# Performance work log

Measured on AMD Instinct MI355X. Metric: run time of the kernel, lower is better.

Reference implementation:

```python
import jax, jax.numpy as jnp
import numpy as np

B, S, D = 4, 2048, 768
H = 12
HD = D // H  # 64
SCALE = HD ** -0.5

def setup_inputs() -> dict:
    key = jax.random.key(0)
    k1, k2, k3 = jax.random.split(key, 3)
    x = jax.random.normal(k1, (B, S, D), dtype=jnp.float32)
    w_qkv = jax.random.normal(k2, (D, 3 * D), dtype=jnp.float32) * (D ** -0.5)
    w_out = jax.random.normal(k3, (D, D), dtype=jnp.float32) * (D ** -0.5)
    b_out = jnp.zeros((D,), dtype=jnp.float32)
    return {"x": x, "w_qkv": w_qkv, "w_out": w_out, "b_out": b_out}

def reference(x, w_qkv, w_out, b_out):
    B_, S_, D_ = x.shape
    # qkv projection (no bias), then 'b s (qkv h d) -> qkv b h s d'
    qkv = (x @ w_qkv).reshape(B_, S_, 3, H, HD).transpose(2, 0, 3, 1, 4)
    q, k, v = qkv[0], qkv[1], qkv[2]  # each [B, H, S, HD]
    att = jnp.einsum('bhxd,bhyd->bhxy', q, k) * SCALE
    att = jax.nn.softmax(att, axis=-1)  # dropout_rate=0 -> identity
    out = jnp.einsum('bhxy,bhyd->bhxd', att, v)
    out = out.transpose(0, 2, 1, 3).reshape(B_, S_, D_)  # 'b h s d -> b s (h d)'
    return out @ w_out + b_out
```

## Files before the change

### kernel.cpp

```cpp
#include <hip/hip_runtime.h>

#define BB 4
#define SS 2048
#define DD 768
#define HH 12
#define HDIM 64

using bf16_t = __bf16;
typedef __bf16 bf16x8 __attribute__((ext_vector_type(8)));
typedef __bf16 bf16x4 __attribute__((ext_vector_type(4)));
typedef float f32x4 __attribute__((ext_vector_type(4)));
typedef unsigned int u32;

static __device__ __forceinline__ void cp16(void* lds, const void* g) {
  __builtin_amdgcn_global_load_lds(
      (const __attribute__((address_space(1))) u32*)g,
      (__attribute__((address_space(3))) u32*)lds, 16, 0, 0);
}

__global__ void cvt_x(const float* __restrict__ in, bf16_t* __restrict__ out) {
  const size_t i = ((size_t)blockIdx.x * 256 + threadIdx.x) * 8;
  f32x4 f0 = *(const f32x4*)(in + i);
  f32x4 f1 = *(const f32x4*)(in + i + 4);
  bf16x8 v;
#pragma unroll
  for (int j = 0; j < 4; j++) { v[j] = (bf16_t)f0[j]; v[4 + j] = (bf16_t)f1[j]; }
  *(bf16x8*)(out + i) = v;
}

__global__ void wt_transpose(const float* __restrict__ in, bf16_t* __restrict__ out,
                             int K, int N) {
  __shared__ bf16_t tile[64][65];
  const int n0 = blockIdx.x * 64, k0 = blockIdx.y * 64;
  const int t = threadIdx.x;
  const int r = t >> 2;
  const int c0 = (t & 3) * 16;
  const float* src = in + (size_t)(k0 + r) * N + n0 + c0;
#pragma unroll
  for (int q = 0; q < 4; q++) {
    f32x4 f = *(const f32x4*)(src + q * 4);
#pragma unroll
    for (int j = 0; j < 4; j++) tile[r][c0 + q * 4 + j] = (bf16_t)f[j];
  }
  __syncthreads();
  bf16x8 o0, o1;
#pragma unroll
  for (int j = 0; j < 8; j++) { o0[j] = tile[c0 + j][r]; o1[j] = tile[c0 + 8 + j][r]; }
  *(bf16x8*)(out + (size_t)(n0 + r) * K + k0 + c0) = o0;
  *(bf16x8*)(out + (size_t)(n0 + r) * K + k0 + c0 + 8) = o1;
}

template <int MODE>
__global__ __launch_bounds__(256, 2)
void gemm_bt(const bf16_t* __restrict__ A, const bf16_t* __restrict__ Bt,
             int M, int N, int K,
             bf16_t* __restrict__ q_out, bf16_t* __restrict__ k_out,
             bf16_t* __restrict__ vt_out,
             float* __restrict__ Cout, const float* __restrict__ bias) {
  __shared__ bf16_t As[2][128][64];
  __shared__ bf16_t Bs[2][128][64];
  const int t = threadIdx.x;
  const int lane = t & 63, wave = t >> 6;
  const int l15 = lane & 15, quad = lane >> 4;
  const int wm = (wave >> 1) * 64, wn = (wave & 1) * 64;

  const int nx = gridDim.x;
  const int L = blockIdx.y * nx + blockIdx.x;
  const int chunk = (nx * gridDim.y) >> 3;
  const int v = (L & 7) * chunk + (L >> 3);
  const int m0 = (v / nx) * 128, n0 = (v % nx) * 128;

  const int srow = lane >> 3;
  const int schunk = ((lane & 7) ^ srow) * 8;
  const int rsw = l15 & 7;

  f32x4 acc[4][4];
#pragma unroll
  for (int i = 0; i < 4; i++)
#pragma unroll
    for (int j = 0; j < 4; j++) acc[i][j] = (f32x4){0.f, 0.f, 0.f, 0.f};

  auto stage = [&](int k0, int buf) {
#pragma unroll
    for (int p = 0; p < 4; p++) {
      const int row = wave * 32 + p * 8 + srow;
      const bf16_t* asrc;
      if (MODE == 0) {
        asrc = A + (size_t)(m0 + row) * K + k0 + schunk;
      } else {
        const int mm = m0 + row, b = mm >> 11, s = mm & 2047, h = k0 >> 6;
        asrc = A + (((size_t)(b * HH + h)) * SS + s) * HDIM + schunk;
      }
      cp16(&As[buf][wave * 32 + p * 8][0], asrc);
      cp16(&Bs[buf][wave * 32 + p * 8][0],
           Bt + (size_t)(n0 + row) * K + k0 + schunk);
    }
  };

  const int NT = K / 64;
  stage(0, 0);

  for (int kt = 0; kt < NT; kt++) {
    const int buf = kt & 1;
    __syncthreads();
    if (kt + 1 < NT) stage((kt + 1) * 64, buf ^ 1);
#pragma unroll
    for (int kk = 0; kk < 2; kk++) {
      bf16x8 af[4], bfr[4];
#pragma unroll
      for (int i = 0; i < 4; i++)
        af[i] = *(const bf16x8*)&As[buf][wm + i * 16 + l15][((kk * 4 + quad) ^ rsw) * 8];
#pragma unroll
      for (int j = 0; j < 4; j++)
        bfr[j] = *(const bf16x8*)&Bs[buf][wn + j * 16 + l15][((kk * 4 + quad) ^ rsw) * 8];
#pragma unroll
      for (int i = 0; i < 4; i++)
#pragma unroll
        for (int j = 0; j < 4; j++)
          acc[i][j] = __builtin_amdgcn_mfma_f32_16x16x32_bf16(af[i], bfr[j], acc[i][j], 0, 0, 0);
    }
  }

  const float QSCALE = 0.125f * 1.44269504088896340736f;
#pragma unroll
  for (int i = 0; i < 4; i++) {
    const int mbase = m0 + wm + i * 16 + quad * 4;
#pragma unroll
    for (int j = 0; j < 4; j++) {
      const int n = n0 + wn + j * 16 + l15;
#pragma unroll
      for (int r = 0; r < 4; r++) {
        const float v = acc[i][j][r];
        const int mm = mbase + r;
        if (MODE == 0) {
          const int sel = n / DD;
          const int rem = n - sel * DD;
          const int h = rem >> 6, d = rem & 63;
          const int b = mm >> 11, s = mm & 2047;
          if (sel == 2) {
            const int sp = (s & ~63) | (((s & 15) << 2) | ((s >> 4) & 3));
            vt_out[((size_t)(b * HH + h) * HDIM + d) * SS + sp] = (bf16_t)v;
          } else {
            const size_t idx = (((size_t)(b * HH + h)) * SS + s) * HDIM + d;
            if (sel == 0) q_out[idx] = (bf16_t)(v * QSCALE);
            else k_out[idx] = (bf16_t)v;
          }
        } else {
          Cout[(size_t)mm * N + n] = v + bias[n];
        }
      }
    }
  }
}

__global__ __launch_bounds__(256, 3)
void attn_kernel(bf16_t* __restrict__ Qio, const bf16_t* __restrict__ Kg,
                 const bf16_t* __restrict__ Vt) {
  __shared__ bf16_t Ks[2][64][64];
  __shared__ bf16_t Vts[2][64][64];
  __shared__ bf16_t Ps[128][64];
  const int t = threadIdx.x;
  const int lane = t & 63, wave = t >> 6;
  const int l15 = lane & 15, quad = lane >> 4;

  const int L = blockIdx.y * gridDim.x + blockIdx.x;
  const int v = (L & 7) * ((16 * BB * HH) / 8) + (L >> 3);
  const int bh = v >> 4;
  const int q0 = (v & 15) * 128;

  const size_t base = (size_t)bh * SS * HDIM;
  const size_t baset = (size_t)bh * HDIM * SS;
  const int wq = wave * 32;
  const int srow = lane >> 3;
  const int schunk = ((lane & 7) ^ srow) * 8;
  const int rsw = l15 & 7;

  bf16x8 qf[2][2];
#pragma unroll
  for (int rt = 0; rt < 2; rt++)
#pragma unroll
    for (int kh = 0; kh < 2; kh++)
      qf[rt][kh] = *(const bf16x8*)(Qio + base + (size_t)(q0 + wq + rt * 16 + l15) * HDIM +
                                    kh * 32 + quad * 8);

  float l_loc[2][4];
  f32x4 o_acc[2][4];
#pragma unroll
  for (int rt = 0; rt < 2; rt++) {
#pragma unroll
    for (int r = 0; r < 4; r++) l_loc[rt][r] = 0.f;
#pragma unroll
    for (int dt = 0; dt < 4; dt++) o_acc[rt][dt] = (f32x4){0.f, 0.f, 0.f, 0.f};
  }

  auto stage = [&](int k0, int buf) {
#pragma unroll
    for (int p = 0; p < 2; p++) {
      const int row = wave * 16 + p * 8 + srow;
      cp16(&Ks[buf][wave * 16 + p * 8][0],
           Kg + base + (size_t)(k0 + row) * HDIM + schunk);
      cp16(&Vts[buf][wave * 16 + p * 8][0],
           Vt + baset + (size_t)row * SS + k0 + schunk);
    }
  };

  stage(0, 0);

  for (int it = 0; it < SS / 64; it++) {
    const int buf = it & 1;
    __syncthreads();

    if (it + 1 < SS / 64) stage((it + 1) * 64, buf ^ 1);

    f32x4 s_acc[2][4];
#pragma unroll
    for (int rt = 0; rt < 2; rt++)
#pragma unroll
      for (int ct = 0; ct < 4; ct++) s_acc[rt][ct] = (f32x4){0.f, 0.f, 0.f, 0.f};
    __builtin_amdgcn_s_setprio(1);
#pragma unroll
    for (int kh = 0; kh < 2; kh++) {
#pragma unroll
      for (int ct = 0; ct < 4; ct++) {
        bf16x8 kf = *(const bf16x8*)&Ks[buf][ct * 16 + l15][((kh * 4 + quad) ^ rsw) * 8];
#pragma unroll
        for (int rt = 0; rt < 2; rt++)
          s_acc[rt][ct] = __builtin_amdgcn_mfma_f32_16x16x32_bf16(qf[rt][kh], kf, s_acc[rt][ct], 0, 0, 0);
      }
    }
    __builtin_amdgcn_s_setprio(0);

#pragma unroll
    for (int rt = 0; rt < 2; rt++) {
#pragma unroll
      for (int r = 0; r < 4; r++) {
        const float p0 = __builtin_amdgcn_exp2f(s_acc[rt][0][r]);
        const float p1 = __builtin_amdgcn_exp2f(s_acc[rt][1][r]);
        const float p2 = __builtin_amdgcn_exp2f(s_acc[rt][2][r]);
        const float p3 = __builtin_amdgcn_exp2f(s_acc[rt][3][r]);
        l_loc[rt][r] += (p0 + p1) + (p2 + p3);
        bf16x4 pk = {(bf16_t)p0, (bf16_t)p1, (bf16_t)p2, (bf16_t)p3};
        const int row = wq + rt * 16 + quad * 4 + r;
        *(bf16x4*)&Ps[row][((l15 >> 1) ^ (row & 7)) * 8 + (l15 & 1) * 4] = pk;
      }
    }

    __builtin_amdgcn_s_setprio(1);
#pragma unroll
    for (int kh = 0; kh < 2; kh++) {
      bf16x8 pf[2];
#pragma unroll
      for (int rt = 0; rt < 2; rt++)
        pf[rt] = *(const bf16x8*)&Ps[wq + rt * 16 + l15][((kh * 4 + quad) ^ rsw) * 8];
#pragma unroll
      for (int dt = 0; dt < 4; dt++) {
        bf16x8 vf = *(const bf16x8*)&Vts[buf][dt * 16 + l15][((kh * 4 + quad) ^ rsw) * 8];
#pragma unroll
        for (int rt = 0; rt < 2; rt++)
          o_acc[rt][dt] = __builtin_amdgcn_mfma_f32_16x16x32_bf16(pf[rt], vf, o_acc[rt][dt], 0, 0, 0);
      }
    }
    __builtin_amdgcn_s_setprio(0);
  }

#pragma unroll
  for (int rt = 0; rt < 2; rt++) {
#pragma unroll
    for (int r = 0; r < 4; r++) {
      float l = l_loc[rt][r];
#pragma unroll
      for (int off = 1; off < 16; off <<= 1) l += __shfl_xor(l, off);
      const float inv = 1.0f / l;
      const int s = q0 + wq + rt * 16 + quad * 4 + r;
#pragma unroll
      for (int dt = 0; dt < 4; dt++) {
        const int d = dt * 16 + l15;
        Qio[base + (size_t)s * HDIM + d] = (bf16_t)(o_acc[rt][dt][r] * inv);
      }
    }
  }
}

extern "C" void kernel_launch(void* const* d_in, const int* in_sizes, int n_in,
                              void* d_out, int out_size, void* d_ws, size_t ws_size,
                              hipStream_t stream) {
  const float* x = (const float*)d_in[0];
  const float* w_qkv = (const float*)d_in[1];
  const float* w_out = (const float*)d_in[2];
  const float* b_out = (const float*)d_in[3];
  float* out = (float*)d_out;

  char* ws = (char*)d_ws;
  bf16_t* wqkv_t = (bf16_t*)ws; ws += (size_t)3 * DD * DD * 2;
  bf16_t* wout_t = (bf16_t*)ws; ws += (size_t)DD * DD * 2;
  bf16_t* q_ws = (bf16_t*)ws;   ws += (size_t)BB * HH * SS * HDIM * 2;
  bf16_t* k_ws = (bf16_t*)ws;
  bf16_t* vt_sc = (bf16_t*)d_out;
  bf16_t* xb = (bf16_t*)d_out + (size_t)BB * SS * DD;

  cvt_x<<<(BB * SS * DD) / (256 * 8), 256, 0, stream>>>(x, xb);
  wt_transpose<<<dim3(3 * DD / 64, DD / 64), 256, 0, stream>>>(w_qkv, wqkv_t, DD, 3 * DD);
  wt_transpose<<<dim3(DD / 64, DD / 64), 256, 0, stream>>>(w_out, wout_t, DD, DD);
  gemm_bt<0><<<dim3(3 * DD / 128, BB * SS / 128), 256, 0, stream>>>(
      xb, wqkv_t, BB * SS, 3 * DD, DD, q_ws, k_ws, vt_sc, nullptr, nullptr);
  attn_kernel<<<dim3(SS / 128, BB * HH), 256, 0, stream>>>(q_ws, k_ws, vt_sc);
  gemm_bt<1><<<dim3(DD / 128, BB * SS / 128), 256, 0, stream>>>(
      q_ws, wout_t, BB * SS, DD, DD, nullptr, nullptr, nullptr, out, b_out);
}
```

Baseline: 223.6 us.

## Use 32x32x16 MFMA with transposed scores and register-resident P via permlane swap

The attention inner loop switches from 16x16x32 to 32x32x16 bf16 MFMA and computes the transposed score tile (K times Q), so each lane holds scores for one query column. The probabilities are repacked in registers with v_permlane32_swap into the A operand of the PV MFMA, which removes the shared-memory round trip through the Ps buffer. The V projection epilogue drops its permuted layout accordingly, and row sums are gathered through a small LDS array at the end. The larger MFMA tile reduces LDS reads per FLOP, but lane-level permutes and the 32-wide accumulator raise register pressure.

```diff
diff --git a/kernel.cpp b/kernel.cpp
--- a/kernel.cpp
+++ b/kernel.cpp
@@ -9,8 +9,11 @@
 using bf16_t = __bf16;
 typedef __bf16 bf16x8 __attribute__((ext_vector_type(8)));
 typedef __bf16 bf16x4 __attribute__((ext_vector_type(4)));
+typedef __bf16 bf16x2 __attribute__((ext_vector_type(2)));
 typedef float f32x4 __attribute__((ext_vector_type(4)));
+typedef float f32x16 __attribute__((ext_vector_type(16)));
 typedef unsigned int u32;
+typedef unsigned int u32x4 __attribute__((ext_vector_type(4)));
 
 static __device__ __forceinline__ void cp16(void* lds, const void* g) {
   __builtin_amdgcn_global_load_lds(
@@ -138,8 +141,7 @@
           const int h = rem >> 6, d = rem & 63;
           const int b = mm >> 11, s = mm & 2047;
           if (sel == 2) {
-            const int sp = (s & ~63) | (((s & 15) << 2) | ((s >> 4) & 3));
-            vt_out[((size_t)(b * HH + h) * HDIM + d) * SS + sp] = (bf16_t)v;
+            vt_out[((size_t)(b * HH + h) * HDIM + d) * SS + s] = (bf16_t)v;
           } else {
             const size_t idx = (((size_t)(b * HH + h)) * SS + s) * HDIM + d;
             if (sel == 0) q_out[idx] = (bf16_t)(v * QSCALE);
@@ -158,10 +160,10 @@
                  const bf16_t* __restrict__ Vt) {
   __shared__ bf16_t Ks[2][64][64];
   __shared__ bf16_t Vts[2][64][64];
-  __shared__ bf16_t Ps[128][64];
+  __shared__ float lsum[128];
   const int t = threadIdx.x;
   const int lane = t & 63, wave = t >> 6;
-  const int l15 = lane & 15, quad = lane >> 4;
+  const int l31 = lane & 31, hi = lane >> 5;
 
   const int L = blockIdx.y * gridDim.x + blockIdx.x;
   const int v = (L & 7) * ((16 * BB * HH) / 8) + (L >> 3);
@@ -173,25 +175,20 @@
   const int wq = wave * 32;
   const int srow = lane >> 3;
   const int schunk = ((lane & 7) ^ srow) * 8;
-  const int rsw = l15 & 7;
-
-  bf16x8 qf[2][2];
-#pragma unroll
-  for (int rt = 0; rt < 2; rt++)
-#pragma unroll
-    for (int kh = 0; kh < 2; kh++)
-      qf[rt][kh] = *(const bf16x8*)(Qio + base + (size_t)(q0 + wq + rt * 16 + l15) * HDIM +
-                                    kh * 32 + quad * 8);
-
-  float l_loc[2][4];
-  f32x4 o_acc[2][4];
-#pragma unroll
-  for (int rt = 0; rt < 2; rt++) {
-#pragma unroll
-    for (int r = 0; r < 4; r++) l_loc[rt][r] = 0.f;
-#pragma unroll
-    for (int dt = 0; dt < 4; dt++) o_acc[rt][dt] = (f32x4){0.f, 0.f, 0.f, 0.f};
-  }
+  const int rsw = l31 & 7;
+
+  bf16x8 qf[4];
+#pragma unroll
+  for (int kd = 0; kd < 4; kd++)
+    qf[kd] = *(const bf16x8*)(Qio + base + (size_t)(q0 + wq + l31) * HDIM +
+                              kd * 16 + hi * 8);
+
+  float l_lane = 0.f;
+  f32x16 o_acc[2];
+#pragma unroll
+  for (int dt = 0; dt < 2; dt++)
+#pragma unroll
+    for (int r = 0; r < 16; r++) o_acc[dt][r] = 0.f;
 
   auto stage = [&](int k0, int buf) {
 #pragma unroll
@@ -209,74 +206,72 @@
   for (int it = 0; it < SS / 64; it++) {
     const int buf = it & 1;
     __syncthreads();
-
     if (it + 1 < SS / 64) stage((it + 1) * 64, buf ^ 1);
 
-    f32x4 s_acc[2][4];
-#pragma unroll
-    for (int rt = 0; rt < 2; rt++)
-#pragma unroll
-      for (int ct = 0; ct < 4; ct++) s_acc[rt][ct] = (f32x4){0.f, 0.f, 0.f, 0.f};
+    f32x16 sT[2];
+#pragma unroll
+    for (int ct = 0; ct < 2; ct++)
+#pragma unroll
+      for (int r = 0; r < 16; r++) sT[ct][r] = 0.f;
     __builtin_amdgcn_s_setprio(1);
 #pragma unroll
-    for (int kh = 0; kh < 2; kh++) {
-#pragma unroll
-      for (int ct = 0; ct < 4; ct++) {
-        bf16x8 kf = *(const bf16x8*)&Ks[buf][ct * 16 + l15][((kh * 4 + quad) ^ rsw) * 8];
-#pragma unroll
-        for (int rt = 0; rt < 2; rt++)
-          s_acc[rt][ct] = __builtin_amdgcn_mfma_f32_16x16x32_bf16(qf[rt][kh], kf, s_acc[rt][ct], 0, 0, 0);
-      }
-    }
+    for (int ct = 0; ct < 2; ct++)
+#pragma unroll
+      for (int kd = 0; kd < 4; kd++) {
+        bf16x8 kf = *(const bf16x8*)&Ks[buf][ct * 32 + l31][((2 * kd + hi) ^ rsw) * 8];
+        sT[ct] = __builtin_amdgcn_mfma_f32_32x32x16_bf16(kf, qf[kd], sT[ct], 0, 0, 0);
+      }
     __builtin_amdgcn_s_setprio(0);
 
-#pragma unroll
-    for (int rt = 0; rt < 2; rt++) {
-#pragma unroll
-      for (int r = 0; r < 4; r++) {
-        const float p0 = __builtin_amdgcn_exp2f(s_acc[rt][0][r]);
-        const float p1 = __builtin_amdgcn_exp2f(s_acc[rt][1][r]);
-        const float p2 = __builtin_amdgcn_exp2f(s_acc[rt][2][r]);
-        const float p3 = __builtin_amdgcn_exp2f(s_acc[rt][3][r]);
-        l_loc[rt][r] += (p0 + p1) + (p2 + p3);
-        bf16x4 pk = {(bf16_t)p0, (bf16_t)p1, (bf16_t)p2, (bf16_t)p3};
-        const int row = wq + rt * 16 + quad * 4 + r;
-        *(bf16x4*)&Ps[row][((l15 >> 1) ^ (row & 7)) * 8 + (l15 & 1) * 4] = pk;
+    bf16x8 pa[4];
+#pragma unroll
+    for (int ct = 0; ct < 2; ct++) {
+      float p[16];
+#pragma unroll
+      for (int r = 0; r < 16; r++) p[r] = __builtin_amdgcn_exp2f(sT[ct][r]);
+#pragma unroll
+      for (int r = 0; r < 16; r += 4)
+        l_lane += (p[r] + p[r + 1]) + (p[r + 2] + p[r + 3]);
+      u32 w[4][2];
+#pragma unroll
+      for (int g = 0; g < 4; g++)
+#pragma unroll
+        for (int i = 0; i < 2; i++) {
+          bf16x2 pk = {(bf16_t)p[4 * g + 2 * i], (bf16_t)p[4 * g + 2 * i + 1]};
+          w[g][i] = *(u32*)&pk;
+        }
+#pragma unroll
+      for (int sub = 0; sub < 2; sub++) {
+        u32 a0 = w[2 * sub][0], b0 = w[2 * sub + 1][0];
+        u32 a1 = w[2 * sub][1], b1 = w[2 * sub + 1][1];
+        asm volatile("v_permlane32_swap_b32 %0, %1" : "+v"(a0), "+v"(b0));
+        asm volatile("v_permlane32_swap_b32 %0, %1" : "+v"(a1), "+v"(b1));
+        u32x4 fr = {a0, a1, b0, b1};
+        pa[ct * 2 + sub] = *(bf16x8*)&fr;
       }
     }
 
     __builtin_amdgcn_s_setprio(1);
 #pragma unroll
-    for (int kh = 0; kh < 2; kh++) {
-      bf16x8 pf[2];
-#pragma unroll
-      for (int rt = 0; rt < 2; rt++)
-        pf[rt] = *(const bf16x8*)&Ps[wq + rt * 16 + l15][((kh * 4 + quad) ^ rsw) * 8];
-#pragma unroll
-      for (int dt = 0; dt < 4; dt++) {
-        bf16x8 vf = *(const bf16x8*)&Vts[buf][dt * 16 + l15][((kh * 4 + quad) ^ rsw) * 8];
-#pragma unroll
-        for (int rt = 0; rt < 2; rt++)
-          o_acc[rt][dt] = __builtin_amdgcn_mfma_f32_16x16x32_bf16(pf[rt], vf, o_acc[rt][dt], 0, 0, 0);
-      }
-    }
+    for (int kk = 0; kk < 4; kk++)
+#pragma unroll
+      for (int dt = 0; dt < 2; dt++) {
+        bf16x8 vf = *(const bf16x8*)&Vts[buf][dt * 32 + l31][((2 * kk + hi) ^ rsw) * 8];
+        o_acc[dt] = __builtin_amdgcn_mfma_f32_32x32x16_bf16(pa[kk], vf, o_acc[dt], 0, 0, 0);
+      }
     __builtin_amdgcn_s_setprio(0);
   }
 
-#pragma unroll
-  for (int rt = 0; rt < 2; rt++) {
-#pragma unroll
-    for (int r = 0; r < 4; r++) {
-      float l = l_loc[rt][r];
-#pragma unroll
-      for (int off = 1; off < 16; off <<= 1) l += __shfl_xor(l, off);
-      const float inv = 1.0f / l;
-      const int s = q0 + wq + rt * 16 + quad * 4 + r;
-#pragma unroll
-      for (int dt = 0; dt < 4; dt++) {
-        const int d = dt * 16 + l15;
-        Qio[base + (size_t)s * HDIM + d] = (bf16_t)(o_acc[rt][dt][r] * inv);
-      }
+  const float lf = l_lane + __shfl_xor(l_lane, 32);
+  lsum[wq + l31] = lf;
+#pragma unroll
+  for (int r = 0; r < 16; r++) {
+    const int q = wq + (r & 3) + 8 * (r >> 2) + 4 * hi;
+    const float inv = 1.0f / lsum[q];
+#pragma unroll
+    for (int dt = 0; dt < 2; dt++) {
+      const int d = dt * 32 + l31;
+      Qio[base + (size_t)(q0 + q) * HDIM + d] = (bf16_t)(o_acc[dt][r] * inv);
     }
   }
 }
```

Result: slower. 228.2 us (+2.1%).
